# Performance work log

Hardware: AMD Instinct MI355X
Metric: run time of the kernel (lower is better)

Reference implementation:

```python
import jax, jax.numpy as jnp
from jax import lax
import numpy as np

B, L, IN_DIM, HID, BINS = 1, 384, 41, 64, 63
ATTN_DIM, NUM_ANCHORS = 32, 32
NUM_CONV, ATTN_EVERY = 6, 2
SIGMA, EPS = 12.0, 1e-5
DILATIONS = [1, 2, 4, 8, 16]


def select_anchors(length, k):
    # deterministic 'stride' mode of select_anchors
    k = max(1, min(k, length))
    stride = max(1, length // k)
    idx = np.arange(0, length, stride)[:k]
    if idx.size < k:
        idx = np.concatenate([idx, np.full(k - idx.size, length - 1)])
    return jnp.asarray(idx, dtype=jnp.int32)


def conv2d(x, w, b, dilation=1):
    # x: (b, Cin, H, W), w: (Cout, Cin, kh, kw) -- 'same' padding like torch padding=dilation*(k//2)
    pad = dilation * (w.shape[-1] // 2)
    y = lax.conv_general_dilated(x, w, (1, 1), [(pad, pad), (pad, pad)],
                                 rhs_dilation=(dilation, dilation),
                                 dimension_numbers=('NCHW', 'OIHW', 'NCHW'))
    return y + b[None, :, None, None]


def instance_norm(x):
    # torch InstanceNorm2d(affine=False), eps=1e-5, per (b, c) over spatial dims
    mu = x.mean(axis=(2, 3), keepdims=True)
    var = x.var(axis=(2, 3), keepdims=True)
    return (x - mu) * lax.rsqrt(var + EPS)


def anchor_attention(pair, td, tq, anchors, wq, wl, wr, wvl, wvr, wo, wg, bg,
                     tg_w1, tg_b1, tg_w2, tg_b2):
    # pair: (b, L, L, d); td: (b, L, L); tq: (b,)
    q = pair @ wq                                    # (b, L, L, a)
    p_left = pair[:, :, anchors, :]                  # (b, L, K, d)
    p_right = pair[:, anchors, :, :]                 # (b, K, L, d)
    left = p_left @ wl                               # (b, L, K, a)
    right = p_right @ wr                             # (b, K, L, a)
    scores = jnp.einsum('bija,bika->bijk', q, left)
    scores = scores + jnp.einsum('bija,bkja->bijk', q, right)
    scores = scores / jnp.sqrt(jnp.float32(ATTN_DIM))
    # template bias, 'consistency' mode
    t_left = td[:, :, anchors]                       # (b, L, K)
    t_right = jnp.swapaxes(td[:, anchors, :], 1, 2)  # (b, L, K)
    t_sum = t_left[:, :, None, :] + t_right[:, None, :, :]  # (b, L, L, K)
    bias = -jnp.abs(t_sum - td[..., None]) / SIGMA
    # TemplateGate
    coverage = (td > 0).astype(jnp.float32).mean(axis=(1, 2))        # (b,)
    length_norm = jnp.full_like(coverage, td.shape[-1] / 512.0)
    feats = jnp.stack([coverage, tq, length_norm], axis=-1)          # (b, 3)
    g = jax.nn.sigmoid(jax.nn.relu(feats @ tg_w1 + tg_b1) @ tg_w2 + tg_b2)  # (b, 1)
    scores = scores + g[:, :, None, None] * bias
    attn = jax.nn.softmax(scores, axis=-1)
    v_left = p_left @ wvl                            # (b, L, K, a)
    v_right = p_right @ wvr                          # (b, K, L, a)
    update = jnp.einsum('bijk,bika->bija', attn, v_left)
    update = update + jnp.einsum('bijk,bkja->bija', attn, v_right)
    update = update @ wo                             # (b, L, L, d)
    gate = jax.nn.sigmoid(pair @ wg + bg)
    return pair + gate * update


def setup_inputs() -> dict:
    key = jax.random.key(0)
    ks = iter(jax.random.split(key, 40))

    def rn(shape, scale=0.05):
        return jax.random.normal(next(ks), shape, dtype=jnp.float32) * scale

    return dict(
        features=jax.random.normal(next(ks), (B, L, L, IN_DIM), dtype=jnp.float32),
        template_dist=jax.random.uniform(next(ks), (B, L, L), dtype=jnp.float32) * 20.0,
        template_quality=jax.random.uniform(next(ks), (B,), dtype=jnp.float32),
        in_w=rn((HID, IN_DIM, 1, 1)), in_b=rn((HID,)),
        conv1_w=rn((NUM_CONV, HID, HID, 3, 3)), conv1_b=rn((NUM_CONV, HID)),
        conv2_w=rn((NUM_CONV, HID, HID, 3, 3)), conv2_b=rn((NUM_CONV, HID)),
        wq=rn((HID, ATTN_DIM)), wl=rn((HID, ATTN_DIM)), wr=rn((HID, ATTN_DIM)),
        wvl=rn((HID, ATTN_DIM)), wvr=rn((HID, ATTN_DIM)), wo=rn((ATTN_DIM, HID)),
        wg=rn((HID, HID)), bg=rn((HID,)),
        tg_w1=rn((3, 16)), tg_b1=rn((16,)), tg_w2=rn((16, 1)), tg_b2=rn((1,)),
        dist_w=rn((BINS, HID, 3, 3)), dist_b=rn((BINS,)),
        cf_w1=rn((32, BINS, 3, 3)), cf_b1=rn((32,)),
        cf_w2=rn((32, 32, 3, 3)), cf_b2=rn((32,)),
        cf_w3=rn((1, 32, 1, 1)), cf_b3=rn((1,)),
    )


def reference(features, template_dist, template_quality, in_w, in_b,
              conv1_w, conv1_b, conv2_w, conv2_b,
              wq, wl, wr, wvl, wvr, wo, wg, bg, tg_w1, tg_b1, tg_w2, tg_b2,
              dist_w, dist_b, cf_w1, cf_b1, cf_w2, cf_b2, cf_w3, cf_b3):
    anchors = select_anchors(L, NUM_ANCHORS)
    x = conv2d(jnp.transpose(features, (0, 3, 1, 2)), in_w, in_b)  # (b, hid, L, L)
    num_attn = max(1, NUM_CONV // max(1, ATTN_EVERY))
    attn_added = 0
    for i in range(NUM_CONV):
        d = DILATIONS[i % len(DILATIONS)]
        res = x
        out = jax.nn.elu(instance_norm(conv2d(x, conv1_w[i], conv1_b[i], d)))
        out = instance_norm(conv2d(out, conv2_w[i], conv2_b[i], 1))
        x = jax.nn.elu(out + res)
        if (i + 1) % ATTN_EVERY == 0 and attn_added < num_attn:
            pair = jnp.transpose(x, (0, 2, 3, 1))
            pair = anchor_attention(pair, template_dist, template_quality, anchors,
                                    wq, wl, wr, wvl, wvr, wo, wg, bg,
                                    tg_w1, tg_b1, tg_w2, tg_b2)
            x = jnp.transpose(pair, (0, 3, 1, 2))
            attn_added += 1
    logits = conv2d(x, dist_w, dist_b)                       # (b, bins, L, L)
    logits = 0.5 * (logits + jnp.swapaxes(logits, 2, 3))     # symmetrize_pairs
    c = jax.nn.relu(conv2d(logits, cf_w1, cf_b1))
    c = jax.nn.relu(conv2d(c, cf_w2, cf_b2))
    confidence = jax.nn.sigmoid(conv2d(c, cf_w3, cf_b3))[:, 0]   # (b, L, L)
    distance_logits = jnp.transpose(logits, (0, 2, 3, 1))        # (b, L, L, bins)
    return distance_logits, confidence
```

## Files before the change

### kernel.cpp

```cpp
#include <hip/hip_runtime.h>
#include <math.h>

#define LDIM 384
#define NPIX (LDIM*LDIM)
#define NBINS 63

typedef __attribute__((ext_vector_type(8))) __bf16 bf16x8;
typedef __attribute__((ext_vector_type(4))) float floatx4;

__device__ __forceinline__ float sigf(float x){ return 1.f/(1.f+expf(-x)); }
__device__ __forceinline__ float elu_neg(float v){ return __expf(v) - 1.f; }

__global__ __launch_bounds__(256) void prep_kernel(
    const float* __restrict__ c1w, const float* __restrict__ c2w,
    const float* __restrict__ dw, const float* __restrict__ cf1w,
    const float* __restrict__ cf2w, const float* __restrict__ wg,
    const float* __restrict__ wo, const float* __restrict__ wq,
    const float* __restrict__ inw, __bf16* __restrict__ Wf){
  int idx = blockIdx.x*256 + threadIdx.x;
  if (idx >= 523264) return;
  if (idx >= 515072){
    int rel = idx - 515072;
    int hi = (rel < 4096) ? 1 : 0;
    int r = rel & 4095;
    int j = r & 7, lane = (r>>3) & 63;
    int r2 = r >> 9;
    int nt = r2 & 3, kc = r2 >> 2;
    int k = kc*32 + (lane>>4)*8 + j;
    int n = nt*16 + (lane&15);
    float v = (k < 41) ? inw[(size_t)n*41 + k] : 0.f;
    __bf16 h = (__bf16)v;
    Wf[idx] = hi ? h : (__bf16)(v - (float)h);
    return;
  }
  if (idx >= 506880){
    int rel, NT, NDIM; const float* src;
    if (idx < 510976){ rel = idx - 506880; src = wg; NT=4; NDIM=64; }
    else if (idx < 513024){ rel = idx - 510976; src = wo; NT=4; NDIM=64; }
    else { rel = idx - 513024; src = wq; NT=2; NDIM=32; }
    int j = rel & 7, lane = (rel>>3) & 63;
    int r2 = rel >> 9;
    int nt = r2 % NT, kc = r2 / NT;
    int k = kc*32 + (lane>>4)*8 + j;
    int n = nt*16 + (lane&15);
    Wf[idx] = (__bf16)src[(size_t)k*NDIM + n];
    return;
  }
  const float* src; int ICreal, OCreal, ICP, NT, rel;
  if (idx < 442368){
    int layer = idx / 36864; rel = idx - layer*36864;
    int i = layer >> 1;
    src = (layer & 1) ? (c2w + (size_t)i*36864) : (c1w + (size_t)i*36864);
    ICreal=64; OCreal=64; ICP=64; NT=4;
  } else if (idx < 479232){
    rel = idx - 442368; src = dw;   ICreal=64; OCreal=63; ICP=64; NT=4;
  } else if (idx < 497664){
    rel = idx - 479232; src = cf1w; ICreal=63; OCreal=32; ICP=64; NT=2;
  } else {
    rel = idx - 497664; src = cf2w; ICreal=32; OCreal=32; ICP=32; NT=2;
  }
  int j = rel & 7, lane = (rel>>3) & 63;
  int r2 = rel >> 9;
  int nt = r2 % NT; int r3 = r2 / NT;
  int KC = ICP/32;
  int kc = r3 % KC; int tap = r3 / KC;
  int k = kc*32 + (lane>>4)*8 + j;
  int n = nt*16 + (lane&15);
  float v = 0.f;
  if (k < ICreal && n < OCreal) v = src[((size_t)n*ICreal + k)*9 + tap];
  Wf[idx] = (__bf16)v;
}

#define VMCNT(N) asm volatile("s_waitcnt vmcnt(%0)" :: "n"(N) : "memory")
#define LGKM0()  asm volatile("s_waitcnt lgkmcnt(0)" ::: "memory")
#define BARS()   { __builtin_amdgcn_s_barrier(); __builtin_amdgcn_sched_barrier(0); }

template<int ICP, int NT, int D, int WAVES>
__global__ __launch_bounds__(WAVES*64) void mfma_conv(
    const __bf16* __restrict__ Ain, const __bf16* __restrict__ Wf,
    const float* __restrict__ bias, int OC_real,
    float* __restrict__ outF, __bf16* __restrict__ outP,
    int relu, float* __restrict__ ostats){
  constexpr int KC = ICP/32;
  constexpr int OCS = NT*16;
  constexpr int REC_B = ICP*4;
  constexpr int PPX = REC_B/16;
  constexpr int HALF = PPX/2;
  constexpr int W = WAVES*16;
  constexpr int T = WAVES*64;
  constexpr int SW = W + 2*D;
  constexpr int TOT1 = SW*PPX;
  constexpr int NITER = (TOT1 + T - 1)/T;
  constexpr int BUFB = NITER*T*16;
  extern __shared__ __align__(16) char smem[];
  char* buf0 = smem;
  char* buf1 = smem + BUFB;
  const int t = threadIdx.x;
  const int wave = t>>6, lane = t&63;
  const int q = lane>>4, col16 = lane&15;
  const int y = blockIdx.y;
  const int x0 = blockIdx.x*W;

  int srcoff[NITER];
  bool oob[NITER];
  #pragma unroll
  for (int k=0;k<NITER;k++){
    int s = k*T + t;
    int px = s / PPX;
    int sub = s % PPX;
    int cg = sub ^ (px & 7);
    int gx = x0 - D + px;
    oob[k] = (px < SW) && ((unsigned)gx >= LDIM);
    int gxc = min(max(gx,0), LDIM-1);
    srcoff[k] = gxc*REC_B + cg*16;
  }

  auto STAGE = [&](char* buf, int ky){
    int yr = y + (ky-1)*D;
    int yc = min(max(yr,0), LDIM-1);
    const char* rb = (const char*)Ain + (size_t)yc*LDIM*REC_B;
    #pragma unroll
    for (int k=0;k<NITER;k++){
      char* ldsb = buf + ((size_t)k*T + wave*64)*16;
      const char* src = rb + srcoff[k];
      __builtin_amdgcn_global_load_lds(
          (const __attribute__((address_space(1))) void*)src,
          (__attribute__((address_space(3))) void*)ldsb, 16, 0, 0);
    }
  };
  auto ZOOB = [&](char* buf){
    #pragma unroll
    for (int k=0;k<NITER;k++)
      if (oob[k]){ uint4 z={0u,0u,0u,0u}; *(uint4*)(buf + ((size_t)k*T + t)*16) = z; }
  };

  floatx4 acc[NT];
  #pragma unroll
  for (int b=0;b<NT;b++){ floatx4 z = {0.f,0.f,0.f,0.f}; acc[b]=z; }

  auto MFMA_PHASE = [&](const char* buf, int ky){
    int yr = y + (ky-1)*D;
    if ((unsigned)yr >= LDIM) return;
    #pragma unroll
    for (int kx=0;kx<3;kx++){
      int cl = wave*16 + col16 + kx*D;
      int e = cl & 7;
      bf16x8 wf[KC][NT];
      #pragma unroll
      for (int kc=0;kc<KC;kc++){
        const __bf16* wkc = Wf + (size_t)((ky*3+kx)*KC + kc)*NT*512 + lane*8;
        #pragma unroll
        for (int nt=0;nt<NT;nt++)
          wf[kc][nt] = *(const bf16x8*)(wkc + (size_t)nt*512);
      }
      #pragma unroll
      for (int kc=0;kc<KC;kc++){
        int sh = (kc*4+q) ^ e;
        int sl = (HALF + kc*4+q) ^ e;
        bf16x8 ah = *(const bf16x8*)(buf + (size_t)cl*REC_B + sh*16);
        bf16x8 al = *(const bf16x8*)(buf + (size_t)cl*REC_B + sl*16);
        #pragma unroll
        for (int nt=0;nt<NT;nt++){
          acc[nt] = __builtin_amdgcn_mfma_f32_16x16x32_bf16(ah, wf[kc][nt], acc[nt], 0,0,0);
          acc[nt] = __builtin_amdgcn_mfma_f32_16x16x32_bf16(al, wf[kc][nt], acc[nt], 0,0,0);
        }
      }
    }
  };

  STAGE(buf0, 0);
  STAGE(buf1, 1);
  VMCNT(NITER);
  ZOOB(buf0); LGKM0();
  BARS();
  MFMA_PHASE(buf0, 0);
  BARS();
  STAGE(buf0, 2);
  VMCNT(NITER);
  ZOOB(buf1); LGKM0();
  BARS();
  MFMA_PHASE(buf1, 1);
  VMCNT(0);
  ZOOB(buf0); LGKM0();
  BARS();
  MFMA_PHASE(buf0, 2);

  float sAcc[NT], sqAcc[NT];
  #pragma unroll
  for (int nt=0;nt<NT;nt++){ sAcc[nt]=0.f; sqAcc[nt]=0.f; }
  #pragma unroll
  for (int nt=0; nt<NT; nt++){
    int oc = nt*16 + col16;
    float bv = (oc < OC_real) ? bias[oc] : 0.f;
    int pxb = x0 + wave*16 + q*4;
    #pragma unroll
    for (int r=0; r<4; r++){
      float vv = acc[nt][r] + bv;
      if (relu) vv = fmaxf(vv, 0.f);
      size_t pix = (size_t)y*LDIM + pxb + r;
      if (outF) outF[pix*OCS + oc] = vv;
      if (outP){
        __bf16 h = (__bf16)vv;
        __bf16* rec = outP + pix*(size_t)(OCS*2);
        rec[oc] = h; rec[OCS+oc] = (__bf16)(vv - (float)h);
      }
      sAcc[nt] += vv; sqAcc[nt] += vv*vv;
    }
  }
  if (ostats){
    float* red = (float*)smem;
    __syncthreads();
    #pragma unroll
    for (int nt=0; nt<NT; nt++){
      int oc = nt*16 + col16;
      float s = sAcc[nt], sq = sqAcc[nt];
      s  += __shfl_xor(s, 16);  s  += __shfl_xor(s, 32);
      sq += __shfl_xor(sq, 16); sq += __shfl_xor(sq, 32);
      if (q == 0){
        red[oc*WAVES + wave] = s;
        red[OCS*WAVES + oc*WAVES + wave] = sq;
      }
    }
    __syncthreads();
    float* oslot = ostats + ((blockIdx.y & 7) << 7);
    if (t < OCS){
      float s=0.f, sq=0.f;
      #pragma unroll
      for (int w=0; w<WAVES; w++){
        s  += red[t*WAVES + w];
        sq += red[OCS*WAVES + t*WAVES + w];
      }
      atomicAdd(&oslot[t], s);
      atomicAdd(&oslot[64+t], sq);
    }
  }
}

__global__ __launch_bounds__(256) void in_proj_mfma(
    const float* __restrict__ feat, const __bf16* __restrict__ WinF,
    const float* __restrict__ b, __bf16* __restrict__ PX){
  const int t=threadIdx.x, wave=t>>6, lane=t&63, q=lane>>4, col16=lane&15;
  const size_t p0=(size_t)blockIdx.x*128;
  floatx4 acc[2][4];
  #pragma unroll
  for (int a=0;a<2;a++)
    #pragma unroll
    for (int c=0;c<4;c++){ floatx4 z={0.f,0.f,0.f,0.f}; acc[a][c]=z; }
  #pragma unroll
  for (int kc=0;kc<2;kc++){
    bf16x8 ah[2], al[2];
    #pragma unroll
    for (int mt=0;mt<2;mt++){
      size_t row = p0 + wave*32 + mt*16 + col16;
      const float* fp = feat + row*41 + kc*32 + q*8;
      float v[8];
      #pragma unroll
      for (int j=0;j<8;j++){
        int k = kc*32 + q*8 + j;
        v[j] = (k < 41) ? fp[j] : 0.f;
      }
      #pragma unroll
      for (int j=0;j<8;j++){
        __bf16 h = (__bf16)v[j];
        ah[mt][j] = h; al[mt][j] = (__bf16)(v[j] - (float)h);
      }
    }
    #pragma unroll
    for (int nt=0;nt<4;nt++){
      bf16x8 bh = *(const bf16x8*)(WinF + (size_t)(kc*4+nt)*512 + lane*8);
      bf16x8 bl = *(const bf16x8*)(WinF + 4096 + (size_t)(kc*4+nt)*512 + lane*8);
      #pragma unroll
      for (int mt=0;mt<2;mt++){
        acc[mt][nt] = __builtin_amdgcn_mfma_f32_16x16x32_bf16(ah[mt], bh, acc[mt][nt], 0,0,0);
        acc[mt][nt] = __builtin_amdgcn_mfma_f32_16x16x32_bf16(al[mt], bh, acc[mt][nt], 0,0,0);
        acc[mt][nt] = __builtin_amdgcn_mfma_f32_16x16x32_bf16(ah[mt], bl, acc[mt][nt], 0,0,0);
      }
    }
  }
  #pragma unroll
  for (int mt=0;mt<2;mt++){
    size_t pxb = p0 + wave*32 + mt*16 + q*4;
    #pragma unroll
    for (int nt=0;nt<4;nt++){
      int oc = nt*16 + col16;
      float bv = b[oc];
      #pragma unroll
      for (int r=0;r<4;r++){
        float vv = acc[mt][nt][r] + bv;
        __bf16* rec = PX + (pxb+r)*128;
        __bf16 h = (__bf16)vv;
        rec[oc] = h; rec[64+oc] = (__bf16)(vv - (float)h);
      }
    }
  }
}

__global__ __launch_bounds__(256) void norm_elu_planes(
    __bf16* __restrict__ U, const float* __restrict__ stats){
  size_t idx = (size_t)blockIdx.x*256 + threadIdx.x;
  size_t px = idx>>3; int c0 = (int)(idx&7)*8;
  __bf16* ur = U + px*128;
  uint4 uh = *(const uint4*)(ur + c0);
  uint4 ul = *(const uint4*)(ur + 64 + c0);
  __bf16* uhp=(__bf16*)&uh; __bf16* ulp=(__bf16*)&ul;
  float mu[8], rs[8];
  #pragma unroll
  for (int k=0;k<8;k++){
    int c = c0+k;
    float s=0.f, sq=0.f;
    #pragma unroll
    for (int rp=0;rp<8;rp++){ s += stats[rp*128 + c]; sq += stats[rp*128 + 64 + c]; }
    float m = s*(1.f/NPIX);
    mu[k]=m; rs[k]=rsqrtf(sq*(1.f/NPIX) - m*m + 1e-5f);
  }
  #pragma unroll
  for (int k=0;k<8;k++){
    float v = ((float)uhp[k] + (float)ulp[k] - mu[k])*rs[k];
    v = v>0.f ? v : elu_neg(v);
    __bf16 h = (__bf16)v; uhp[k]=h; ulp[k]=(__bf16)(v-(float)h);
  }
  *(uint4*)(ur + c0) = uh;
  *(uint4*)(ur + 64 + c0) = ul;
}

__global__ __launch_bounds__(256) void norm_res_elu_planes(
    const __bf16* __restrict__ U, __bf16* __restrict__ PX,
    const float* __restrict__ stats){
  size_t idx = (size_t)blockIdx.x*256 + threadIdx.x;
  size_t px = idx>>3; int c0 = (int)(idx&7)*8;
  const __bf16* ur = U + px*128;
  __bf16* xr = PX + px*128;
  uint4 uh = *(const uint4*)(ur + c0);
  uint4 ul = *(const uint4*)(ur + 64 + c0);
  uint4 xh = *(uint4*)(xr + c0);
  uint4 xl = *(uint4*)(xr + 64 + c0);
  __bf16* uhp=(__bf16*)&uh; __bf16* ulp=(__bf16*)&ul;
  __bf16* xhp=(__bf16*)&xh; __bf16* xlp=(__bf16*)&xl;
  float mu[8], rs[8];
  #pragma unroll
  for (int k=0;k<8;k++){
    int c = c0+k;
    float s=0.f, sq=0.f;
    #pragma unroll
    for (int rp=0;rp<8;rp++){ s += stats[rp*128 + c]; sq += stats[rp*128 + 64 + c]; }
    float m = s*(1.f/NPIX);
    mu[k]=m; rs[k]=rsqrtf(sq*(1.f/NPIX) - m*m + 1e-5f);
  }
  #pragma unroll
  for (int k=0;k<8;k++){
    float v = ((float)uhp[k] + (float)ulp[k] - mu[k])*rs[k]
            + ((float)xhp[k] + (float)xlp[k]);
    v = v>0.f ? v : elu_neg(v);
    __bf16 h = (__bf16)v; xhp[k]=h; xlp[k]=(__bf16)(v-(float)h);
  }
  *(uint4*)(xr + c0) = xh;
  *(uint4*)(xr + 64 + c0) = xl;
}

__global__ __launch_bounds__(256) void g_partial_kernel(
    const float* __restrict__ td, float* __restrict__ GC){
  size_t base = (size_t)blockIdx.x*256;
  float cnt = (td[base + threadIdx.x] > 0.f) ? 1.f : 0.f;
  __shared__ float red[256];
  red[threadIdx.x]=cnt; __syncthreads();
  for (int st=128; st; st>>=1){
    if (threadIdx.x<st) red[threadIdx.x]+=red[threadIdx.x+st];
    __syncthreads();
  }
  if (threadIdx.x==0) atomicAdd(GC, red[0]);
}

__global__ void g_final_kernel(
    const float* __restrict__ GC, const float* __restrict__ tq,
    const float* __restrict__ w1, const float* __restrict__ b1,
    const float* __restrict__ w2, const float* __restrict__ b2,
    float* __restrict__ G){
  if (threadIdx.x==0){
    float f0 = GC[0]*(1.f/NPIX), f1 = tq[0], f2 = (float)LDIM/512.f;
    float z = b2[0];
    for (int j=0;j<16;j++){
      float h = f0*w1[j] + f1*w1[16+j] + f2*w1[32+j] + b1[j];
      z += (h>0.f?h:0.f)*w2[j];
    }
    G[0] = sigf(z);
  }
}

__global__ __launch_bounds__(256) void qproj_mfma_kernel(
    const __bf16* __restrict__ PX, const __bf16* __restrict__ WqF,
    __bf16* __restrict__ Qb){
  const int t=threadIdx.x, wave=t>>6, lane=t&63, q=lane>>4, col16=lane&15;
  const size_t p0=(size_t)blockIdx.x*128;
  __shared__ __bf16 Xhi[128*72];
  __shared__ __bf16 Xlo[128*72];
  uint4 sv[8];
  #pragma unroll
  for (int k=0;k<8;k++){
    int c=t+k*256;
    sv[k] = *(const uint4*)((const char*)PX + (p0 + (c>>4))*256 + (c&15)*16);
  }
  #pragma unroll
  for (int k=0;k<8;k++){
    int c=t+k*256; int px=c>>4, sub=c&15;
    *(uint4*)(((sub<8)?Xhi:Xlo) + px*72 + (sub&7)*8) = sv[k];
  }
  __syncthreads();
  floatx4 acc[2][2];
  #pragma unroll
  for (int a=0;a<2;a++)
    #pragma unroll
    for (int b=0;b<2;b++){ floatx4 z={0.f,0.f,0.f,0.f}; acc[a][b]=z; }
  #pragma unroll
  for (int kc=0;kc<2;kc++){
    bf16x8 ah[2], al[2];
    #pragma unroll
    for (int mt=0;mt<2;mt++){
      int row = wave*32 + mt*16 + col16;
      ah[mt] = *(const bf16x8*)(Xhi + row*72 + kc*32 + q*8);
      al[mt] = *(const bf16x8*)(Xlo + row*72 + kc*32 + q*8);
    }
    #pragma unroll
    for (int nt=0;nt<2;nt++){
      bf16x8 b = *(const bf16x8*)(WqF + (kc*2+nt)*512 + lane*8);
      acc[0][nt] = __builtin_amdgcn_mfma_f32_16x16x32_bf16(ah[0], b, acc[0][nt], 0,0,0);
      acc[1][nt] = __builtin_amdgcn_mfma_f32_16x16x32_bf16(ah[1], b, acc[1][nt], 0,0,0);
      acc[0][nt] = __builtin_amdgcn_mfma_f32_16x16x32_bf16(al[0], b, acc[0][nt], 0,0,0);
      acc[1][nt] = __builtin_amdgcn_mfma_f32_16x16x32_bf16(al[1], b, acc[1][nt], 0,0,0);
    }
  }
  #pragma unroll
  for (int mt=0;mt<2;mt++){
    size_t pxb = p0 + wave*32 + mt*16 + q*4;
    #pragma unroll
    for (int nt=0;nt<2;nt++){
      int oc = nt*16 + col16;
      #pragma unroll
      for (int r=0;r<4;r++)
        Qb[(pxb+r)*32 + oc] = (__bf16)acc[mt][nt][r];
    }
  }
}

__global__ __launch_bounds__(256) void proj_left_kernel(
    const __bf16* __restrict__ PX, const float* __restrict__ wl, const float* __restrict__ wvl,
    __bf16* __restrict__ leftb, __bf16* __restrict__ vleftTb){
  int i = blockIdx.x;
  __shared__ float xa[32][65];
  __shared__ float w1s[2048], w2s[2048];
  int c = threadIdx.x & 63;
  for (int a = threadIdx.x>>6; a<32; a+=4){
    const __bf16* rec = PX + ((size_t)i*LDIM + 12*a)*128;
    xa[a][c] = (float)rec[c] + (float)rec[64+c];
  }
  for (int idx=threadIdx.x; idx<2048; idx+=256){ w1s[idx]=wl[idx]; w2s[idx]=wvl[idx]; }
  __syncthreads();
  #pragma unroll
  for (int k=0;k<4;k++){
    int idx = threadIdx.x + k*256;
    int a = idx>>5, n = idx&31;
    float a1=0.f, a2=0.f;
    #pragma unroll
    for (int cc=0;cc<64;cc++){ float v=xa[a][cc]; a1+=v*w1s[cc*32+n]; a2+=v*w2s[cc*32+n]; }
    leftb  [(size_t)i*1024 + a*32 + n] = (__bf16)a1;
    vleftTb[(size_t)i*1024 + n*32 + a] = (__bf16)a2;
  }
}

__global__ __launch_bounds__(256) void proj_right_kernel(
    const __bf16* __restrict__ PX, const float* __restrict__ wr, const float* __restrict__ wvr,
    __bf16* __restrict__ rightb, __bf16* __restrict__ vrightTb){
  int a = blockIdx.y; int row = 12*a;
  int j0 = blockIdx.x*32;
  __shared__ float xr[32][65];
  __shared__ float w1s[2048], w2s[2048];
  for (int idx=threadIdx.x; idx<2048; idx+=256){ w1s[idx]=wr[idx]; w2s[idx]=wvr[idx]; }
  int c = threadIdx.x & 63;
  for (int jl = threadIdx.x>>6; jl<32; jl+=4){
    const __bf16* rec = PX + ((size_t)row*LDIM + j0 + jl)*128;
    xr[jl][c] = (float)rec[c] + (float)rec[64+c];
  }
  __syncthreads();
  #pragma unroll
  for (int k=0;k<4;k++){
    int idx=threadIdx.x+k*256; int jl=idx>>5, n=idx&31;
    float a1=0.f, a2=0.f;
    #pragma unroll
    for (int cc=0;cc<64;cc++){ float v=xr[jl][cc]; a1+=v*w1s[cc*32+n]; a2+=v*w2s[cc*32+n]; }
    rightb  [(size_t)(j0+jl)*1024 + a*32 + n] = (__bf16)a1;
    vrightTb[(size_t)(j0+jl)*1024 + n*32 + a] = (__bf16)a2;
  }
}

__global__ __launch_bounds__(256) void attn_s1_kernel(
    const __bf16* __restrict__ Qb, const __bf16* __restrict__ leftb,
    float* __restrict__ S){
  const int t=threadIdx.x, wave=t>>6, lane=t&63, q=lane>>4, col16=lane&15;
  const int i = blockIdx.y, j0 = blockIdx.x*128;
  bf16x8 bfrag[2];
  #pragma unroll
  for (int nt=0;nt<2;nt++)
    bfrag[nt] = *(const bf16x8*)(leftb + (size_t)i*1024 + (nt*16+col16)*32 + q*8);
  bf16x8 ah[2];
  #pragma unroll
  for (int mt=0;mt<2;mt++){
    int row = j0 + wave*32 + mt*16 + col16;
    ah[mt] = *(const bf16x8*)(Qb + ((size_t)i*LDIM + row)*32 + q*8);
  }
  floatx4 acc[2][2];
  #pragma unroll
  for (int a=0;a<2;a++)
    #pragma unroll
    for (int b=0;b<2;b++){ floatx4 z={0.f,0.f,0.f,0.f}; acc[a][b]=z; }
  #pragma unroll
  for (int mt=0;mt<2;mt++)
    #pragma unroll
    for (int nt=0;nt<2;nt++)
      acc[mt][nt] = __builtin_amdgcn_mfma_f32_16x16x32_bf16(ah[mt], bfrag[nt], acc[mt][nt], 0,0,0);
  #pragma unroll
  for (int mt=0;mt<2;mt++){
    int jb = j0 + wave*32 + mt*16 + q*4;
    #pragma unroll
    for (int nt=0;nt<2;nt++){
      int a = nt*16 + col16;
      #pragma unroll
      for (int r=0;r<4;r++)
        S[((size_t)i*LDIM + jb + r)*32 + a] = acc[mt][nt][r];
    }
  }
}

__global__ __launch_bounds__(256) void attn_s2_kernel(
    const __bf16* __restrict__ Qb, const __bf16* __restrict__ rightb,
    float* __restrict__ S){
  const int t=threadIdx.x, wave=t>>6, lane=t&63, q=lane>>4, col16=lane&15;
  const int j = blockIdx.y, i0 = blockIdx.x*128;
  bf16x8 bfrag[2];
  #pragma unroll
  for (int nt=0;nt<2;nt++)
    bfrag[nt] = *(const bf16x8*)(rightb + (size_t)j*1024 + (nt*16+col16)*32 + q*8);
  bf16x8 ah[2];
  #pragma unroll
  for (int mt=0;mt<2;mt++){
    int row = i0 + wave*32 + mt*16 + col16;
    ah[mt] = *(const bf16x8*)(Qb + ((size_t)row*LDIM + j)*32 + q*8);
  }
  floatx4 acc[2][2];
  #pragma unroll
  for (int a=0;a<2;a++)
    #pragma unroll
    for (int b=0;b<2;b++){ floatx4 z={0.f,0.f,0.f,0.f}; acc[a][b]=z; }
  #pragma unroll
  for (int mt=0;mt<2;mt++)
    #pragma unroll
    for (int nt=0;nt<2;nt++)
      acc[mt][nt] = __builtin_amdgcn_mfma_f32_16x16x32_bf16(ah[mt], bfrag[nt], acc[mt][nt], 0,0,0);
  #pragma unroll
  for (int mt=0;mt<2;mt++){
    int ib = i0 + wave*32 + mt*16 + q*4;
    #pragma unroll
    for (int nt=0;nt<2;nt++){
      int a = nt*16 + col16;
      #pragma unroll
      for (int r=0;r<4;r++){
        size_t idx = ((size_t)(ib+r)*LDIM + j)*32 + a;
        S[idx] += acc[mt][nt][r];
      }
    }
  }
}

__global__ __launch_bounds__(128) void attn_soft_kernel(
    const float* __restrict__ S, const float* __restrict__ td,
    const float* __restrict__ gp, __bf16* __restrict__ attnb,
    __bf16* __restrict__ attnTb){
  int i = blockIdx.y;
  int j0 = blockIdx.x*128;
  int t = threadIdx.x;
  int j = j0 + t;
  __shared__ float tl[32];
  __shared__ float trS[32*128];
  {
    #pragma unroll
    for (int v=0; v<8; v++){
      int f = t + v*128;
      int a = f>>5, jl4 = (f&31)*4;
      *(floatx4*)(trS + a*128 + jl4) = *(const floatx4*)(td + (size_t)(12*a)*LDIM + j0 + jl4);
    }
    if (t<32) tl[t] = td[(size_t)i*LDIM + 12*t];
  }
  __syncthreads();
  float g = gp[0];
  float tdij = td[(size_t)i*LDIM+j];
  float s[32];
  const floatx4* sp4 = (const floatx4*)(S + ((size_t)i*LDIM+j)*32);
  #pragma unroll
  for (int v=0;v<8;v++){
    floatx4 sv = sp4[v];
    #pragma unroll
    for (int e=0;e<4;e++) s[v*4+e] = sv[e];
  }
  float m = -1e30f;
  #pragma unroll
  for (int a=0;a<32;a++){
    float acc = s[a]*0.17677669529663687f;
    float bias = -fabsf(tl[a] + trS[a*128 + t] - tdij) * (1.0f/12.0f);
    acc += g*bias;
    s[a]=acc;
    m = fmaxf(m, acc);
  }
  float sum=0.f;
  #pragma unroll
  for (int a=0;a<32;a++){ s[a]=expf(s[a]-m); sum+=s[a]; }
  float inv = 1.f/sum;
  bf16x8 pk[4];
  #pragma unroll
  for (int v=0;v<4;v++){
    #pragma unroll
    for (int e=0;e<8;e++) pk[v][e] = (__bf16)(s[v*8+e]*inv);
  }
  bf16x8* op = (bf16x8*)(attnb + ((size_t)i*LDIM+j)*32);
  bf16x8* opT = (bf16x8*)(attnTb + ((size_t)j*LDIM+i)*32);
  #pragma unroll
  for (int v=0;v<4;v++){ op[v]=pk[v]; opT[v]=pk[v]; }
}

__global__ __launch_bounds__(256) void attn_u1_kernel(
    const __bf16* __restrict__ attnb, const __bf16* __restrict__ vleftTb,
    float* __restrict__ UPD){
  const int t=threadIdx.x, wave=t>>6, lane=t&63, q=lane>>4, col16=lane&15;
  const int i = blockIdx.y, j0 = blockIdx.x*128;
  bf16x8 bfrag[2];
  #pragma unroll
  for (int nt=0;nt<2;nt++)
    bfrag[nt] = *(const bf16x8*)(vleftTb + (size_t)i*1024 + (nt*16+col16)*32 + q*8);
  bf16x8 ah[2];
  #pragma unroll
  for (int mt=0;mt<2;mt++){
    int row = j0 + wave*32 + mt*16 + col16;
    ah[mt] = *(const bf16x8*)(attnb + ((size_t)i*LDIM + row)*32 + q*8);
  }
  floatx4 acc[2][2];
  #pragma unroll
  for (int a=0;a<2;a++)
    #pragma unroll
    for (int b=0;b<2;b++){ floatx4 z={0.f,0.f,0.f,0.f}; acc[a][b]=z; }
  #pragma unroll
  for (int mt=0;mt<2;mt++)
    #pragma unroll
    for (int nt=0;nt<2;nt++)
      acc[mt][nt] = __builtin_amdgcn_mfma_f32_16x16x32_bf16(ah[mt], bfrag[nt], acc[mt][nt], 0,0,0);
  #pragma unroll
  for (int mt=0;mt<2;mt++){
    int jb = j0 + wave*32 + mt*16 + q*4;
    #pragma unroll
    for (int nt=0;nt<2;nt++){
      int c = nt*16 + col16;
      #pragma unroll
      for (int r=0;r<4;r++)
        UPD[((size_t)i*LDIM + jb + r)*32 + c] = acc[mt][nt][r];
    }
  }
}

__global__ __launch_bounds__(256) void attn_u2_kernel(
    const __bf16* __restrict__ attnTb, const __bf16* __restrict__ vrightTb,
    float* __restrict__ UPD){
  const int t=threadIdx.x, wave=t>>6, lane=t&63, q=lane>>4, col16=lane&15;
  const int j = blockIdx.y, i0 = blockIdx.x*128;
  bf16x8 bfrag[2];
  #pragma unroll
  for (int nt=0;nt<2;nt++)
    bfrag[nt] = *(const bf16x8*)(vrightTb + (size_t)j*1024 + (nt*16+col16)*32 + q*8);
  bf16x8 ah[2];
  #pragma unroll
  for (int mt=0;mt<2;mt++){
    int row = i0 + wave*32 + mt*16 + col16;
    ah[mt] = *(const bf16x8*)(attnTb + ((size_t)j*LDIM + row)*32 + q*8);
  }
  floatx4 acc[2][2];
  #pragma unroll
  for (int a=0;a<2;a++)
    #pragma unroll
    for (int b=0;b<2;b++){ floatx4 z={0.f,0.f,0.f,0.f}; acc[a][b]=z; }
  #pragma unroll
  for (int mt=0;mt<2;mt++)
    #pragma unroll
    for (int nt=0;nt<2;nt++)
      acc[mt][nt] = __builtin_amdgcn_mfma_f32_16x16x32_bf16(ah[mt], bfrag[nt], acc[mt][nt], 0,0,0);
  #pragma unroll
  for (int mt=0;mt<2;mt++){
    int ib = i0 + wave*32 + mt*16 + q*4;
    #pragma unroll
    for (int nt=0;nt<2;nt++){
      int c = nt*16 + col16;
      #pragma unroll
      for (int r=0;r<4;r++){
        size_t idx = ((size_t)(ib+r)*LDIM + j)*32 + c;
        UPD[idx] += acc[mt][nt][r];
      }
    }
  }
}

__global__ __launch_bounds__(256) void gate_mfma_kernel(
    __bf16* __restrict__ PX, const float* __restrict__ UPD,
    const __bf16* __restrict__ WgF, const __bf16* __restrict__ WoF,
    const float* __restrict__ bg){
  const int t=threadIdx.x, wave=t>>6, lane=t&63, q=lane>>4, col16=lane&15;
  const size_t p0=(size_t)blockIdx.x*128;
  __shared__ __bf16 Xhi[128*72];
  __shared__ __bf16 Xlo[128*72];
  __shared__ __bf16 Ub[128*40];
  uint4 sv[8];
  #pragma unroll
  for (int k=0;k<8;k++){
    int c=t+k*256;
    sv[k] = *(const uint4*)((const char*)PX + (p0 + (c>>4))*256 + (c&15)*16);
  }
  floatx4 uv[4];
  #pragma unroll
  for (int k=0;k<4;k++){
    int p = (t>>3) + k*32;
    uv[k] = *(const floatx4*)(UPD + (p0+p)*32 + (t&7)*4);
  }
  #pragma unroll
  for (int k=0;k<8;k++){
    int c=t+k*256; int px=c>>4, sub=c&15;
    *(uint4*)(((sub<8)?Xhi:Xlo) + px*72 + (sub&7)*8) = sv[k];
  }
  #pragma unroll
  for (int k=0;k<4;k++){
    int p = (t>>3) + k*32;
    __bf16* pu = Ub + p*40 + (t&7)*4;
    #pragma unroll
    for (int kk=0;kk<4;kk++) pu[kk]=(__bf16)uv[k][kk];
  }
  __syncthreads();
  floatx4 accg[2][4], accu[2][4];
  #pragma unroll
  for (int a=0;a<2;a++)
    #pragma unroll
    for (int b=0;b<4;b++){ floatx4 z={0.f,0.f,0.f,0.f}; accg[a][b]=z; accu[a][b]=z; }
  #pragma unroll
  for (int kc=0;kc<2;kc++){
    bf16x8 ah[2], al[2];
    #pragma unroll
    for (int mt=0;mt<2;mt++){
      int row = wave*32 + mt*16 + col16;
      ah[mt] = *(const bf16x8*)(Xhi + row*72 + kc*32 + q*8);
      al[mt] = *(const bf16x8*)(Xlo + row*72 + kc*32 + q*8);
    }
    #pragma unroll
    for (int nt=0;nt<4;nt++){
      bf16x8 b = *(const bf16x8*)(WgF + (kc*4+nt)*512 + lane*8);
      accg[0][nt] = __builtin_amdgcn_mfma_f32_16x16x32_bf16(ah[0], b, accg[0][nt], 0,0,0);
      accg[1][nt] = __builtin_amdgcn_mfma_f32_16x16x32_bf16(ah[1], b, accg[1][nt], 0,0,0);
      accg[0][nt] = __builtin_amdgcn_mfma_f32_16x16x32_bf16(al[0], b, accg[0][nt], 0,0,0);
      accg[1][nt] = __builtin_amdgcn_mfma_f32_16x16x32_bf16(al[1], b, accg[1][nt], 0,0,0);
    }
  }
  {
    bf16x8 au[2];
    #pragma unroll
    for (int mt=0;mt<2;mt++){
      int row = wave*32 + mt*16 + col16;
      au[mt] = *(const bf16x8*)(Ub + row*40 + q*8);
    }
    #pragma unroll
    for (int nt=0;nt<4;nt++){
      bf16x8 b = *(const bf16x8*)(WoF + nt*512 + lane*8);
      accu[0][nt] = __builtin_amdgcn_mfma_f32_16x16x32_bf16(au[0], b, accu[0][nt], 0,0,0);
      accu[1][nt] = __builtin_amdgcn_mfma_f32_16x16x32_bf16(au[1], b, accu[1][nt], 0,0,0);
    }
  }
  #pragma unroll
  for (int mt=0;mt<2;mt++){
    size_t pxb = p0 + wave*32 + mt*16 + q*4;
    #pragma unroll
    for (int nt=0;nt<4;nt++){
      int oc = nt*16 + col16;
      float bgv = bg[oc];
      #pragma unroll
      for (int r=0;r<4;r++){
        __bf16* rec = PX + (pxb+r)*128;
        float xv = (float)rec[oc] + (float)rec[64+oc];
        float g = sigf(accg[mt][nt][r] + bgv);
        float xn = xv + g*accu[mt][nt][r];
        __bf16 h = (__bf16)xn;
        rec[oc] = h; rec[64+oc] = (__bf16)(xn - (float)h);
      }
    }
  }
}

__global__ __launch_bounds__(256) void sym_kernel(
    const float* __restrict__ lg, __bf16* __restrict__ PS, float* __restrict__ dout){
  int i = blockIdx.y;
  int j = blockIdx.x*4 + (threadIdx.x>>6);
  int o = threadIdx.x & 63;
  float v = 0.5f*(lg[((size_t)i*LDIM+j)*64+o] + lg[((size_t)j*LDIM+i)*64+o]);
  size_t pix = (size_t)i*LDIM+j;
  __bf16 h = (__bf16)v;
  __bf16* rec = PS + pix*128;
  rec[o] = h; rec[64+o] = (__bf16)(v - (float)h);
  if (o<63) dout[pix*63+o] = v;
}

__global__ __launch_bounds__(256) void conf_kernel(
    const float* __restrict__ c2, const float* __restrict__ w,
    const float* __restrict__ b, float* __restrict__ out){
  int t = threadIdx.x;
  size_t pix = (size_t)blockIdx.x*8 + (t>>5);
  int c = t&31;
  float v = c2[pix*32 + c]*w[c];
  #pragma unroll
  for (int off=16; off; off>>=1) v += __shfl_xor(v, off);
  if (c==0) out[pix] = sigf(v + b[0]);
}

extern "C" void kernel_launch(void* const* d_in, const int* in_sizes, int n_in,
                              void* d_out, int out_size, void* d_ws, size_t ws_size,
                              hipStream_t stream){
  const float* feat = (const float*)d_in[0];
  const float* td   = (const float*)d_in[1];
  const float* tq   = (const float*)d_in[2];
  const float* in_w = (const float*)d_in[3];
  const float* in_b = (const float*)d_in[4];
  const float* c1w  = (const float*)d_in[5];
  const float* c1b  = (const float*)d_in[6];
  const float* c2w  = (const float*)d_in[7];
  const float* c2b  = (const float*)d_in[8];
  const float* wq   = (const float*)d_in[9];
  const float* wl   = (const float*)d_in[10];
  const float* wr   = (const float*)d_in[11];
  const float* wvl  = (const float*)d_in[12];
  const float* wvr  = (const float*)d_in[13];
  const float* wo   = (const float*)d_in[14];
  const float* wg   = (const float*)d_in[15];
  const float* bg   = (const float*)d_in[16];
  const float* tgw1 = (const float*)d_in[17];
  const float* tgb1 = (const float*)d_in[18];
  const float* tgw2 = (const float*)d_in[19];
  const float* tgb2 = (const float*)d_in[20];
  const float* dw   = (const float*)d_in[21];
  const float* db   = (const float*)d_in[22];
  const float* cf1w = (const float*)d_in[23];
  const float* cf1b = (const float*)d_in[24];
  const float* cf2w = (const float*)d_in[25];
  const float* cf2b = (const float*)d_in[26];
  const float* cf3w = (const float*)d_in[27];
  const float* cf3b = (const float*)d_in[28];

  float* ws = (float*)d_ws;
  const size_t BUF = (size_t)64*NPIX;
  float* R1 = ws;
  float* R2 = ws + BUF;
  float* R3 = ws + 2*BUF;
  float* STATS = ws + 3*BUF;
  float* G     = STATS + 12288;
  float* GC    = G + 1;
  __bf16* WF   = (__bf16*)(G + 16);
  __bf16* WGF  = WF + 506880;
  __bf16* WOF  = WF + 510976;
  __bf16* WQF  = WF + 513024;
  __bf16* WINF = WF + 515072;

  __bf16* PX = (__bf16*)R1;
  __bf16* PT = (__bf16*)R2;
  __bf16* PU = (__bf16*)R3;
  char* R2c = (char*)R2;
  __bf16* Qb       = (__bf16*)R2c;
  __bf16* ATTNB    = (__bf16*)(R2c +  9437184);
  __bf16* ATTNTB   = (__bf16*)(R2c + 18874368);
  __bf16* LEFTB    = (__bf16*)(R2c + 28311552);
  __bf16* RIGHTB   = (__bf16*)(R2c + 29097984);
  __bf16* VLEFTTB  = (__bf16*)(R2c + 29884416);
  __bf16* VRIGHTTB = (__bf16*)(R2c + 30670848);
  float* S   = R3;
  float* UPD = R3 + (size_t)32*NPIX;

  hipMemsetAsync(STATS, 0, (12288 + 16)*sizeof(float), stream);
  prep_kernel<<<2044, 256, 0, stream>>>(c1w, c2w, dw, cf1w, cf2w, wg, wo, wq, in_w, WF);
  g_partial_kernel<<<576, 256, 0, stream>>>(td, GC);
  g_final_kernel<<<1, 64, 0, stream>>>(GC, tq, tgw1, tgb1, tgw2, tgb2, G);

  in_proj_mfma<<<1152, 256, 0, stream>>>(feat, WINF, in_b, PX);

#define CONV_SMEM(ICP_, DD, WW) \
  (2 * (((((WW)*16+2*(DD))*((ICP_)/4)) + ((WW)*64) - 1)/((WW)*64)) * ((WW)*64) * 16)

#define CONV2_NORM(i) \
  norm_elu_planes<<<4608, 256, 0, stream>>>(PT, STATS + (2*(i))*1024); \
  mfma_conv<64,4,1,4><<<dim3(6,LDIM), 256, CONV_SMEM(64,1,4), stream>>>( \
      PT, WF + (size_t)(2*(i)+1)*36864, c2b + (i)*64, 64, \
      nullptr, PU, 0, STATS + (2*(i)+1)*1024); \
  norm_res_elu_planes<<<4608, 256, 0, stream>>>(PU, PX, STATS + (2*(i)+1)*1024);

#define CONV1(i, DD) \
  mfma_conv<64,4,DD,4><<<dim3(6,LDIM), 256, CONV_SMEM(64,DD,4), stream>>>( \
      PX, WF + (size_t)(2*(i))*36864, c1b + (i)*64, 64, \
      nullptr, PT, 0, STATS + (2*(i))*1024);

#define ATTN_BLOCK \
  qproj_mfma_kernel<<<1152, 256, 0, stream>>>(PX, WQF, Qb); \
  proj_left_kernel<<<384, 256, 0, stream>>>(PX, wl, wvl, LEFTB, VLEFTTB); \
  proj_right_kernel<<<dim3(12,32), 256, 0, stream>>>(PX, wr, wvr, RIGHTB, VRIGHTTB); \
  attn_s1_kernel<<<dim3(3,LDIM), 256, 0, stream>>>(Qb, LEFTB, S); \
  attn_s2_kernel<<<dim3(3,LDIM), 256, 0, stream>>>(Qb, RIGHTB, S); \
  attn_soft_kernel<<<dim3(3,LDIM), 128, 0, stream>>>(S, td, G, ATTNB, ATTNTB); \
  attn_u1_kernel<<<dim3(3,LDIM), 256, 0, stream>>>(ATTNB, VLEFTTB, UPD); \
  attn_u2_kernel<<<dim3(3,LDIM), 256, 0, stream>>>(ATTNTB, VRIGHTTB, UPD); \
  gate_mfma_kernel<<<1152, 256, 0, stream>>>(PX, UPD, WGF, WOF, bg);

  CONV1(0, 1)   CONV2_NORM(0)
  CONV1(1, 2)   CONV2_NORM(1)  ATTN_BLOCK
  CONV1(2, 4)   CONV2_NORM(2)
  CONV1(3, 8)   CONV2_NORM(3)  ATTN_BLOCK
  CONV1(4, 16)  CONV2_NORM(4)
  CONV1(5, 1)   CONV2_NORM(5)  ATTN_BLOCK

  mfma_conv<64,4,1,4><<<dim3(6,LDIM), 256, CONV_SMEM(64,1,4), stream>>>(
      PX, WF + 442368, db, 63, R3, nullptr, 0, nullptr);
  sym_kernel<<<dim3(96,LDIM), 256, 0, stream>>>(R3, PT, (float*)d_out);
  mfma_conv<64,2,1,4><<<dim3(6,LDIM), 256, CONV_SMEM(64,1,4), stream>>>(
      PT, WF + 479232, cf1b, 32, nullptr, PX, 1, nullptr);
  mfma_conv<32,2,1,4><<<dim3(6,LDIM), 256, CONV_SMEM(32,1,4), stream>>>(
      PX, WF + 497664, cf2b, 32, R3, nullptr, 1, nullptr);
  conf_kernel<<<18432, 256, 0, stream>>>(R3, cf3w, cf3b, (float*)d_out + (size_t)NPIX*NBINS);
}
```

Before: 1.419 ms.

## Remap conv blocks per XCD and write transposed attention partials instead of scattered accumulates

The conv kernels now launch on a 1D grid and remap block IDs so that each of the 8 XCDs handles a contiguous band of rows, which should improve L2 reuse of the overlapping halo rows. The attention s2 and u2 kernels no longer read-modify-write S/UPD with strided scatter. They write coalesced transposed buffers instead, and the softmax and gate kernels add the two partials on read. This removes the strided RMW traffic at the cost of one extra buffer and one strided gather in the gate kernel.

```diff
diff --git a/kernel.cpp b/kernel.cpp
--- a/kernel.cpp
+++ b/kernel.cpp
@@ -88,6 +88,7 @@
   constexpr int HALF = PPX/2;
   constexpr int W = WAVES*16;
   constexpr int T = WAVES*64;
+  constexpr int NXB = LDIM/W;
   constexpr int SW = W + 2*D;
   constexpr int TOT1 = SW*PPX;
   constexpr int NITER = (TOT1 + T - 1)/T;
@@ -98,8 +99,11 @@
   const int t = threadIdx.x;
   const int wave = t>>6, lane = t&63;
   const int q = lane>>4, col16 = lane&15;
-  const int y = blockIdx.y;
-  const int x0 = blockIdx.x*W;
+  const int bid = blockIdx.x;
+  const int xcd = bid & 7, loc = bid >> 3;
+  const int yl = loc / NXB, xb = loc - yl*NXB;
+  const int y = xcd*(LDIM/8) + yl;
+  const int x0 = xb*W;
 
   int srcoff[NITER];
   bool oob[NITER];
@@ -222,7 +226,7 @@
       }
     }
     __syncthreads();
-    float* oslot = ostats + ((blockIdx.y & 7) << 7);
+    float* oslot = ostats + ((y & 7) << 7);
     if (t < OCS){
       float s=0.f, sq=0.f;
       #pragma unroll
@@ -531,7 +535,7 @@
 
 __global__ __launch_bounds__(256) void attn_s2_kernel(
     const __bf16* __restrict__ Qb, const __bf16* __restrict__ rightb,
-    float* __restrict__ S){
+    float* __restrict__ S2T){
   const int t=threadIdx.x, wave=t>>6, lane=t&63, q=lane>>4, col16=lane&15;
   const int j = blockIdx.y, i0 = blockIdx.x*128;
   bf16x8 bfrag[2];
@@ -561,18 +565,16 @@
     for (int nt=0;nt<2;nt++){
       int a = nt*16 + col16;
       #pragma unroll
-      for (int r=0;r<4;r++){
-        size_t idx = ((size_t)(ib+r)*LDIM + j)*32 + a;
-        S[idx] += acc[mt][nt][r];
-      }
+      for (int r=0;r<4;r++)
+        S2T[((size_t)j*LDIM + ib + r)*32 + a] = acc[mt][nt][r];
     }
   }
 }
 
 __global__ __launch_bounds__(128) void attn_soft_kernel(
-    const float* __restrict__ S, const float* __restrict__ td,
-    const float* __restrict__ gp, __bf16* __restrict__ attnb,
-    __bf16* __restrict__ attnTb){
+    const float* __restrict__ S, const float* __restrict__ S2T,
+    const float* __restrict__ td, const float* __restrict__ gp,
+    __bf16* __restrict__ attnb, __bf16* __restrict__ attnTb){
   int i = blockIdx.y;
   int j0 = blockIdx.x*128;
   int t = threadIdx.x;
@@ -593,11 +595,13 @@
   float tdij = td[(size_t)i*LDIM+j];
   float s[32];
   const floatx4* sp4 = (const floatx4*)(S + ((size_t)i*LDIM+j)*32);
+  const floatx4* sp4b = (const floatx4*)(S2T + ((size_t)j*LDIM+i)*32);
   #pragma unroll
   for (int v=0;v<8;v++){
     floatx4 sv = sp4[v];
-    #pragma unroll
-    for (int e=0;e<4;e++) s[v*4+e] = sv[e];
+    floatx4 sv2 = sp4b[v];
+    #pragma unroll
+    for (int e=0;e<4;e++) s[v*4+e] = sv[e] + sv2[e];
   }
   float m = -1e30f;
   #pragma unroll
@@ -664,7 +668,7 @@
 
 __global__ __launch_bounds__(256) void attn_u2_kernel(
     const __bf16* __restrict__ attnTb, const __bf16* __restrict__ vrightTb,
-    float* __restrict__ UPD){
+    float* __restrict__ UPD2T){
   const int t=threadIdx.x, wave=t>>6, lane=t&63, q=lane>>4, col16=lane&15;
   const int j = blockIdx.y, i0 = blockIdx.x*128;
   bf16x8 bfrag[2];
@@ -694,16 +698,15 @@
     for (int nt=0;nt<2;nt++){
       int c = nt*16 + col16;
       #pragma unroll
-      for (int r=0;r<4;r++){
-        size_t idx = ((size_t)(ib+r)*LDIM + j)*32 + c;
-        UPD[idx] += acc[mt][nt][r];
-      }
+      for (int r=0;r<4;r++)
+        UPD2T[((size_t)j*LDIM + ib + r)*32 + c] = acc[mt][nt][r];
     }
   }
 }
 
 __global__ __launch_bounds__(256) void gate_mfma_kernel(
     __bf16* __restrict__ PX, const float* __restrict__ UPD,
+    const float* __restrict__ UPD2T,
     const __bf16* __restrict__ WgF, const __bf16* __restrict__ WoF,
     const float* __restrict__ bg){
   const int t=threadIdx.x, wave=t>>6, lane=t&63, q=lane>>4, col16=lane&15;
@@ -720,8 +723,13 @@
   floatx4 uv[4];
   #pragma unroll
   for (int k=0;k<4;k++){
-    int p = (t>>3) + k*32;
-    uv[k] = *(const floatx4*)(UPD + (p0+p)*32 + (t&7)*4);
+    size_t p = p0 + (t>>3) + k*32;
+    size_t tp = (p % LDIM)*LDIM + p / LDIM;
+    floatx4 a = *(const floatx4*)(UPD + p*32 + (t&7)*4);
+    floatx4 b = *(const floatx4*)(UPD2T + tp*32 + (t&7)*4);
+    #pragma unroll
+    for (int e=0;e<4;e++) a[e] += b[e];
+    uv[k] = a;
   }
   #pragma unroll
   for (int k=0;k<8;k++){
@@ -876,8 +884,10 @@
   __bf16* RIGHTB   = (__bf16*)(R2c + 29097984);
   __bf16* VLEFTTB  = (__bf16*)(R2c + 29884416);
   __bf16* VRIGHTTB = (__bf16*)(R2c + 30670848);
-  float* S   = R3;
-  float* UPD = R3 + (size_t)32*NPIX;
+  float* S     = R3;
+  float* S2T   = R3 + (size_t)32*NPIX;
+  float* UPD   = R3;
+  float* UPD2T = R3 + (size_t)32*NPIX;
 
   hipMemsetAsync(STATS, 0, (12288 + 16)*sizeof(float), stream);
   prep_kernel<<<2044, 256, 0, stream>>>(c1w, c2w, dw, cf1w, cf2w, wg, wo, wq, in_w, WF);
@@ -891,13 +901,13 @@
 
 #define CONV2_NORM(i) \
   norm_elu_planes<<<4608, 256, 0, stream>>>(PT, STATS + (2*(i))*1024); \
-  mfma_conv<64,4,1,4><<<dim3(6,LDIM), 256, CONV_SMEM(64,1,4), stream>>>( \
+  mfma_conv<64,4,1,4><<<2304, 256, CONV_SMEM(64,1,4), stream>>>( \
       PT, WF + (size_t)(2*(i)+1)*36864, c2b + (i)*64, 64, \
       nullptr, PU, 0, STATS + (2*(i)+1)*1024); \
   norm_res_elu_planes<<<4608, 256, 0, stream>>>(PU, PX, STATS + (2*(i)+1)*1024);
 
 #define CONV1(i, DD) \
-  mfma_conv<64,4,DD,4><<<dim3(6,LDIM), 256, CONV_SMEM(64,DD,4), stream>>>( \
+  mfma_conv<64,4,DD,4><<<2304, 256, CONV_SMEM(64,DD,4), stream>>>( \
       PX, WF + (size_t)(2*(i))*36864, c1b + (i)*64, 64, \
       nullptr, PT, 0, STATS + (2*(i))*1024);
 
@@ -906,11 +916,11 @@
   proj_left_kernel<<<384, 256, 0, stream>>>(PX, wl, wvl, LEFTB, VLEFTTB); \
   proj_right_kernel<<<dim3(12,32), 256, 0, stream>>>(PX, wr, wvr, RIGHTB, VRIGHTTB); \
   attn_s1_kernel<<<dim3(3,LDIM), 256, 0, stream>>>(Qb, LEFTB, S); \
-  attn_s2_kernel<<<dim3(3,LDIM), 256, 0, stream>>>(Qb, RIGHTB, S); \
-  attn_soft_kernel<<<dim3(3,LDIM), 128, 0, stream>>>(S, td, G, ATTNB, ATTNTB); \
+  attn_s2_kernel<<<dim3(3,LDIM), 256, 0, stream>>>(Qb, RIGHTB, S2T); \
+  attn_soft_kernel<<<dim3(3,LDIM), 128, 0, stream>>>(S, S2T, td, G, ATTNB, ATTNTB); \
   attn_u1_kernel<<<dim3(3,LDIM), 256, 0, stream>>>(ATTNB, VLEFTTB, UPD); \
-  attn_u2_kernel<<<dim3(3,LDIM), 256, 0, stream>>>(ATTNTB, VRIGHTTB, UPD); \
-  gate_mfma_kernel<<<1152, 256, 0, stream>>>(PX, UPD, WGF, WOF, bg);
+  attn_u2_kernel<<<dim3(3,LDIM), 256, 0, stream>>>(ATTNTB, VRIGHTTB, UPD2T); \
+  gate_mfma_kernel<<<1152, 256, 0, stream>>>(PX, UPD, UPD2T, WGF, WOF, bg);
 
   CONV1(0, 1)   CONV2_NORM(0)
   CONV1(1, 2)   CONV2_NORM(1)  ATTN_BLOCK
@@ -919,12 +929,12 @@
   CONV1(4, 16)  CONV2_NORM(4)
   CONV1(5, 1)   CONV2_NORM(5)  ATTN_BLOCK
 
-  mfma_conv<64,4,1,4><<<dim3(6,LDIM), 256, CONV_SMEM(64,1,4), stream>>>(
+  mfma_conv<64,4,1,4><<<2304, 256, CONV_SMEM(64,1,4), stream>>>(
       PX, WF + 442368, db, 63, R3, nullptr, 0, nullptr);
   sym_kernel<<<dim3(96,LDIM), 256, 0, stream>>>(R3, PT, (float*)d_out);
-  mfma_conv<64,2,1,4><<<dim3(6,LDIM), 256, CONV_SMEM(64,1,4), stream>>>(
+  mfma_conv<64,2,1,4><<<2304, 256, CONV_SMEM(64,1,4), stream>>>(
       PT, WF + 479232, cf1b, 32, nullptr, PX, 1, nullptr);
-  mfma_conv<32,2,1,4><<<dim3(6,LDIM), 256, CONV_SMEM(32,1,4), stream>>>(
+  mfma_conv<32,2,1,4><<<2304, 256, CONV_SMEM(32,1,4), stream>>>(
       PX, WF + 497664, cf2b, 32, R3, nullptr, 1, nullptr);
   conf_kernel<<<18432, 256, 0, stream>>>(R3, cf3w, cf3b, (float*)d_out + (size_t)NPIX*NBINS);
 }
```

Measured after the change: 1.465 ms. +3.3%, slower.
